# Optimization experiments

Measured on AMD Instinct MI355X. Metric: run time of the kernel, lower is better.

Reference implementation:

```python
import jax, jax.numpy as jnp
import numpy as np

LOWER = 300  # hidden size of the critic MLP


def setup_inputs() -> dict:
    key = jax.random.key(0)
    ks = jax.random.split(key, 6)
    N, XD, YD = 1024, 768, 768
    x = jax.random.normal(ks[0], (N, XD), dtype=jnp.float32)
    y = jax.random.normal(ks[1], (N, YD), dtype=jnp.float32)
    # Linear(x_dim+y_dim -> LOWER), Linear(LOWER -> 1); Kaiming-uniform-ish init
    b1_lim = 1.0 / np.sqrt(XD + YD)
    b2_lim = 1.0 / np.sqrt(LOWER)
    W1 = jax.random.uniform(ks[2], (XD + YD, LOWER), jnp.float32, -b1_lim, b1_lim)
    b1 = jax.random.uniform(ks[3], (LOWER,), jnp.float32, -b1_lim, b1_lim)
    W2 = jax.random.uniform(ks[4], (LOWER, 1), jnp.float32, -b2_lim, b2_lim)
    b2 = jax.random.uniform(ks[5], (1,), jnp.float32, -b2_lim, b2_lim)
    return {"x_samples": x, "y_samples": y, "W1": W1, "b1": b1, "W2": W2, "b2": b2}


def reference(x_samples, y_samples, W1, b1, W2, b2):
    N = y_samples.shape[0]
    xd = x_samples.shape[-1]
    # Decompose first Linear: cat([x, y]) @ W1 == x @ W1[:xd] + y @ W1[xd:]
    Wx, Wy = W1[:xd], W1[xd:]
    hx = x_samples @ Wx          # [N, LOWER]
    hy = y_samples @ Wy          # [N, LOWER]
    w2 = W2[:, 0]                # [LOWER]

    def critic(h):
        # relu -> Linear(LOWER->1) -> softplus
        return jax.nn.softplus(jax.nn.relu(h) @ w2 + b2[0])

    # T0[i] = F(x[i], y[i])
    T0 = critic(hx + hy + b1)                       # [N]
    # T1[i, j] = F(x[j], y[i])  (x tiled over dim 0, y over dim 1)
    h_pair = hy[:, None, :] + hx[None, :, :] + b1   # [N, N, LOWER]
    T1 = critic(h_pair)                             # [N, N]
    lower_bound = (T0.mean()
                   - jax.nn.logsumexp(T1, axis=1).mean()
                   - jnp.log(jnp.float32(N)))
    return lower_bound
```

## Files before the change

kernel.cpp:

```cpp
#include <hip/hip_runtime.h>
#include <math.h>

#define N_S 1024
#define XD  768
#define LOW 300
#define KP  320
#define KP2 160

typedef _Float16 h2  __attribute__((ext_vector_type(2)));
typedef __fp16   g2  __attribute__((ext_vector_type(2)));
typedef _Float16 v8h __attribute__((ext_vector_type(8)));
typedef float    f4  __attribute__((ext_vector_type(4)));

union U32H2 { unsigned int u; h2 h; };
__device__ inline h2 u2h(unsigned int v){ U32H2 t; t.u = v; return t.h; }
__device__ inline unsigned int pk(float a, float b){
    g2 t = __builtin_amdgcn_cvt_pkrtz(a, b);
    return __builtin_bit_cast(unsigned int, t);
}
union U4V8 { uint4 u; v8h v; };

__global__ __launch_bounds__(512)
void gemm_h(const float* __restrict__ x, const float* __restrict__ y,
            const float* __restrict__ W1, const float* __restrict__ b1g,
            unsigned int* __restrict__ hx_h, unsigned int* __restrict__ hy_h,
            float* __restrict__ partsum, unsigned int* __restrict__ cnt)
{
    __shared__ unsigned int As[2][32][36];
    __shared__ unsigned int Bs[2][64][36];

    const int tid = threadIdx.x;
    const int job = blockIdx.x;
    if (job < 256 && tid < 4) partsum[job * 4 + tid] = 0.f;
    if (job == 0 && tid == 4) cnt[0] = 0u;

    const int which = job >= 160;
    const int t = which ? job - 160 : job;
    const int n0 = (t % 5) * 64;
    const int r0 = (t / 5) * 32;
    const float* A = which ? y : x;
    const float* W = W1 + (size_t)which * XD * LOW;
    _Float16* outh = (_Float16*)(which ? hy_h : hx_h);

    const int w = tid >> 6, l = tid & 63;
    const int wm = w >> 2, wn = w & 3;
    const int lr = l & 15, lg = l >> 4;

    const int arow = tid >> 4, aq = tid & 15;
    const int bn = tid & 63, bms = tid >> 6;
    const bool bin = (n0 + bn) < LOW;

    f4 acc = {};
    float4 a0; float bw[8];
    a0 = *(const float4*)&A[(size_t)(r0 + arow) * XD + aq * 4];
    #pragma unroll
    for (int s = 0; s < 8; ++s)
        bw[s] = bin ? W[(size_t)(bms * 8 + s) * LOW + n0 + bn] : 0.f;

    const int NC = XD / 64;
    for (int c = 0; c < NC; ++c) {
        const int buf = c & 1;
        *(uint2*)&As[buf][arow][aq * 2] = make_uint2(pk(a0.x, a0.y), pk(a0.z, a0.w));
        *(uint4*)&Bs[buf][bn][bms * 4] =
            uint4{ pk(bw[0],bw[1]), pk(bw[2],bw[3]), pk(bw[4],bw[5]), pk(bw[6],bw[7]) };
        __syncthreads();
        if (c + 1 < NC) {
            const int kb = (c + 1) * 64;
            a0 = *(const float4*)&A[(size_t)(r0 + arow) * XD + kb + aq * 4];
            #pragma unroll
            for (int s = 0; s < 8; ++s)
                bw[s] = bin ? W[(size_t)(kb + bms * 8 + s) * LOW + n0 + bn] : 0.f;
        }
        #pragma unroll
        for (int ks = 0; ks < 2; ++ks) {
            const int ko = ks * 16 + lg * 4;
            U4V8 af; af.u = *(const uint4*)&As[buf][wm * 16 + lr][ko];
            U4V8 bf; bf.u = *(const uint4*)&Bs[buf][wn * 16 + lr][ko];
            acc = __builtin_amdgcn_mfma_f32_16x16x32_f16(af.v, bf.v, acc, 0, 0, 0);
        }
    }

    const int col = n0 + wn * 16 + lr;
    const float b1v = (which && col < LOW) ? b1g[col] : 0.f;
    #pragma unroll
    for (int r = 0; r < 4; ++r) {
        const int row = r0 + wm * 16 + lg * 4 + r;
        outh[(size_t)row * KP + col] = (_Float16)(acc[r] + b1v);
    }
}

__global__ __launch_bounds__(256)
void pair_kernel(const unsigned int* __restrict__ hx_h, const unsigned int* __restrict__ hy_h,
                 const float* __restrict__ W2, const float* __restrict__ b2,
                 float* __restrict__ partsum, float* __restrict__ diag,
                 unsigned int* __restrict__ cnt, float* __restrict__ out)
{
    const int jb = blockIdx.x & 15, ib = blockIdx.x >> 4;
    const int j0 = jb * 64, i0 = ib * 32;

    __shared__ unsigned int Hy[160][36];
    __shared__ unsigned int Hx[160][68];
    __shared__ unsigned int w2s[KP2];
    __shared__ unsigned int lastFlag;
    __shared__ float ssum[4];

    const int tid = threadIdx.x;

    {
        const int r = tid >> 3, q = tid & 7;
        const unsigned int* src = &hy_h[(size_t)(i0 + r) * KP2];
        #pragma unroll
        for (int e = 0; e < 5; ++e) {
            const int k4 = q + 8 * e;
            uint4 v = *(const uint4*)&src[k4 * 4];
            Hy[k4*4+0][r] = v.x; Hy[k4*4+1][r] = v.y;
            Hy[k4*4+2][r] = v.z; Hy[k4*4+3][r] = v.w;
        }
    }
    {
        const int r = tid >> 2, q = tid & 3;
        const unsigned int* src = &hx_h[(size_t)(j0 + r) * KP2];
        #pragma unroll
        for (int e = 0; e < 10; ++e) {
            const int k4 = q + 4 * e;
            uint4 v = *(const uint4*)&src[k4 * 4];
            Hx[k4*4+0][r] = v.x; Hx[k4*4+1][r] = v.y;
            Hx[k4*4+2][r] = v.z; Hx[k4*4+3][r] = v.w;
        }
    }
    if (tid < KP2) {
        int k = tid * 2;
        float w0 = (k < LOW) ? W2[k] : 0.f;
        float w1 = (k + 1 < LOW) ? W2[k + 1] : 0.f;
        w2s[tid] = pk(w0, w1);
    }
    __syncthreads();

    const int tx = tid & 15;
    const int kh = (tid >> 4) & 1;
    const int iy = tid >> 5;

    float acc[4][4] = {};
    const h2 hz = h2{(_Float16)0.f, (_Float16)0.f};
    const int kbase = kh * 80;

    #pragma unroll 4
    for (int kki = 0; kki < 80; ++kki) {
        const int kk = kbase + kki;
        const uint4 ya = *(const uint4*)&Hy[kk][iy * 4];
        const uint4 xb = *(const uint4*)&Hx[kk][tx * 4];
        const h2 w = u2h(w2s[kk]);
        const unsigned int yar[4] = {ya.x, ya.y, ya.z, ya.w};
        const unsigned int xbr[4] = {xb.x, xb.y, xb.z, xb.w};
        #pragma unroll
        for (int r = 0; r < 4; ++r) {
            const h2 a = u2h(yar[r]);
            #pragma unroll
            for (int q = 0; q < 4; ++q) {
                h2 z = __builtin_elementwise_max(a + u2h(xbr[q]), hz);
                acc[r][q] = __builtin_amdgcn_fdot2(z, w, acc[r][q], false);
            }
        }
    }

    #pragma unroll
    for (int r = 0; r < 4; ++r)
        #pragma unroll
        for (int q = 0; q < 4; ++q)
            acc[r][q] += __shfl_xor(acc[r][q], 16, 64);

    const float b2v = b2[0];
    #pragma unroll
    for (int r = 0; r < 4; ++r) {
        const int row = i0 + iy * 4 + r;
        float es = 0.f;
        #pragma unroll
        for (int q = 0; q < 4; ++q) {
            const float s = acc[r][q] + b2v;
            es += __expf(s);
            const int col = j0 + tx * 4 + q;
            if (col == row)
                atomicExch(&diag[row],
                           fmaxf(s, 0.f) + __logf(1.f + __expf(-fabsf(s))));
        }
        #pragma unroll
        for (int o = 1; o <= 8; o <<= 1) es += __shfl_xor(es, o, 64);
        if ((tid & 31) == 0) atomicAdd(&partsum[row], es);
    }

    asm volatile("s_waitcnt vmcnt(0)" ::: "memory");
    __syncthreads();
    if (tid == 0) lastFlag = (atomicAdd(cnt, 1u) == 511u) ? 1u : 0u;
    __syncthreads();
    if (!lastFlag) return;

    float csum = 0.f;
    #pragma unroll
    for (int g = 0; g < 4; ++g) {
        const int row = g * 256 + tid;
        const float ps = atomicAdd(&partsum[row], 0.f);
        const float dg = atomicAdd(&diag[row], 0.f);
        csum += dg - __logf((float)N_S + ps);
    }
    #pragma unroll
    for (int o = 32; o > 0; o >>= 1) csum += __shfl_xor(csum, o, 64);
    if ((tid & 63) == 0) ssum[tid >> 6] = csum;
    __syncthreads();
    if (tid == 0)
        out[0] = (ssum[0] + ssum[1] + ssum[2] + ssum[3]) * (1.0f / N_S)
               - logf((float)N_S);
}

extern "C" void kernel_launch(void* const* d_in, const int* in_sizes, int n_in,
                              void* d_out, int out_size, void* d_ws, size_t ws_size,
                              hipStream_t stream)
{
    const float* x  = (const float*)d_in[0];
    const float* y  = (const float*)d_in[1];
    const float* W1 = (const float*)d_in[2];
    const float* b1 = (const float*)d_in[3];
    const float* W2 = (const float*)d_in[4];
    const float* b2 = (const float*)d_in[5];
    float* outp = (float*)d_out;

    unsigned int* hx_h = (unsigned int*)d_ws;
    unsigned int* hy_h = hx_h + (size_t)N_S * KP2;
    float* partsum = (float*)(hy_h + (size_t)N_S * KP2);
    float* diag = partsum + N_S;
    unsigned int* cnt = (unsigned int*)(diag + N_S);

    gemm_h<<<320, 512, 0, stream>>>(x, y, W1, b1, hx_h, hy_h, partsum, cnt);

    pair_kernel<<<512, 256, 0, stream>>>(hx_h, hy_h, W2, b2,
                                         partsum, diag, cnt, outp);
}
```

Before: 41.29 us.

## Process two j-tiles per pair block, prefetching the next Hx tile into registers

Each pair_kernel block now covers two 64-column j tiles, so the grid shrinks from 512 to 256 blocks. The Hy tile and W2 load are reused across both tiles. The second Hx tile is loaded from global into registers while the first tile is being computed, overlapping load latency with compute. With 256 blocks on a 256-CU part, each CU gets one block, so there is less parallelism and less latency hiding across blocks, and the added registers for the prefetch may lower occupancy.

```diff
diff --git a/kernel.cpp b/kernel.cpp
--- a/kernel.cpp
+++ b/kernel.cpp
@@ -95,8 +95,9 @@
                  float* __restrict__ partsum, float* __restrict__ diag,
                  unsigned int* __restrict__ cnt, float* __restrict__ out)
 {
-    const int jb = blockIdx.x & 15, ib = blockIdx.x >> 4;
-    const int j0 = jb * 64, i0 = ib * 32;
+    const int jp = blockIdx.x & 7;
+    const int ib = blockIdx.x >> 3;
+    const int i0 = ib * 32;
 
     __shared__ unsigned int Hy[160][36];
     __shared__ unsigned int Hx[160][68];
@@ -117,80 +118,94 @@
             Hy[k4*4+2][r] = v.z; Hy[k4*4+3][r] = v.w;
         }
     }
-    {
-        const int r = tid >> 2, q = tid & 3;
-        const unsigned int* src = &hx_h[(size_t)(j0 + r) * KP2];
-        #pragma unroll
-        for (int e = 0; e < 10; ++e) {
-            const int k4 = q + 4 * e;
-            uint4 v = *(const uint4*)&src[k4 * 4];
-            Hx[k4*4+0][r] = v.x; Hx[k4*4+1][r] = v.y;
-            Hx[k4*4+2][r] = v.z; Hx[k4*4+3][r] = v.w;
-        }
-    }
     if (tid < KP2) {
         int k = tid * 2;
         float w0 = (k < LOW) ? W2[k] : 0.f;
         float w1 = (k + 1 < LOW) ? W2[k + 1] : 0.f;
         w2s[tid] = pk(w0, w1);
     }
-    __syncthreads();
+
+    const int xr = tid >> 2, xq = tid & 3;
+    uint4 xv[10];
+    {
+        const unsigned int* src = &hx_h[(size_t)(jp * 128 + xr) * KP2];
+        #pragma unroll
+        for (int e = 0; e < 10; ++e)
+            xv[e] = *(const uint4*)&src[(xq + 4 * e) * 4];
+    }
 
     const int tx = tid & 15;
     const int kh = (tid >> 4) & 1;
     const int iy = tid >> 5;
-
-    float acc[4][4] = {};
+    const float b2v = b2[0];
     const h2 hz = h2{(_Float16)0.f, (_Float16)0.f};
-    const int kbase = kh * 80;
-
-    #pragma unroll 4
-    for (int kki = 0; kki < 80; ++kki) {
-        const int kk = kbase + kki;
-        const uint4 ya = *(const uint4*)&Hy[kk][iy * 4];
-        const uint4 xb = *(const uint4*)&Hx[kk][tx * 4];
-        const h2 w = u2h(w2s[kk]);
-        const unsigned int yar[4] = {ya.x, ya.y, ya.z, ya.w};
-        const unsigned int xbr[4] = {xb.x, xb.y, xb.z, xb.w};
+
+    for (int jt = 0; jt < 2; ++jt) {
+        const int j0 = (jp * 2 + jt) * 64;
+        if (jt) __syncthreads();
+        #pragma unroll
+        for (int e = 0; e < 10; ++e) {
+            const int k4 = xq + 4 * e;
+            Hx[k4*4+0][xr] = xv[e].x; Hx[k4*4+1][xr] = xv[e].y;
+            Hx[k4*4+2][xr] = xv[e].z; Hx[k4*4+3][xr] = xv[e].w;
+        }
+        __syncthreads();
+        if (jt == 0) {
+            const unsigned int* src = &hx_h[(size_t)(jp * 128 + 64 + xr) * KP2];
+            #pragma unroll
+            for (int e = 0; e < 10; ++e)
+                xv[e] = *(const uint4*)&src[(xq + 4 * e) * 4];
+        }
+
+        float acc[4][4] = {};
+        const int kbase = kh * 80;
+        #pragma unroll 4
+        for (int kki = 0; kki < 80; ++kki) {
+            const int kk = kbase + kki;
+            const uint4 ya = *(const uint4*)&Hy[kk][iy * 4];
+            const uint4 xb = *(const uint4*)&Hx[kk][tx * 4];
+            const h2 w = u2h(w2s[kk]);
+            const unsigned int yar[4] = {ya.x, ya.y, ya.z, ya.w};
+            const unsigned int xbr[4] = {xb.x, xb.y, xb.z, xb.w};
+            #pragma unroll
+            for (int r = 0; r < 4; ++r) {
+                const h2 a = u2h(yar[r]);
+                #pragma unroll
+                for (int q = 0; q < 4; ++q) {
+                    h2 z = __builtin_elementwise_max(a + u2h(xbr[q]), hz);
+                    acc[r][q] = __builtin_amdgcn_fdot2(z, w, acc[r][q], false);
+                }
+            }
+        }
+
+        #pragma unroll
+        for (int r = 0; r < 4; ++r)
+            #pragma unroll
+            for (int q = 0; q < 4; ++q)
+                acc[r][q] += __shfl_xor(acc[r][q], 16, 64);
+
         #pragma unroll
         for (int r = 0; r < 4; ++r) {
-            const h2 a = u2h(yar[r]);
+            const int row = i0 + iy * 4 + r;
+            float es = 0.f;
             #pragma unroll
             for (int q = 0; q < 4; ++q) {
-                h2 z = __builtin_elementwise_max(a + u2h(xbr[q]), hz);
-                acc[r][q] = __builtin_amdgcn_fdot2(z, w, acc[r][q], false);
+                const float s = acc[r][q] + b2v;
+                es += __expf(s);
+                const int col = j0 + tx * 4 + q;
+                if (col == row)
+                    atomicExch(&diag[row],
+                               fmaxf(s, 0.f) + __logf(1.f + __expf(-fabsf(s))));
             }
-        }
-    }
-
-    #pragma unroll
-    for (int r = 0; r < 4; ++r)
-        #pragma unroll
-        for (int q = 0; q < 4; ++q)
-            acc[r][q] += __shfl_xor(acc[r][q], 16, 64);
-
-    const float b2v = b2[0];
-    #pragma unroll
-    for (int r = 0; r < 4; ++r) {
-        const int row = i0 + iy * 4 + r;
-        float es = 0.f;
-        #pragma unroll
-        for (int q = 0; q < 4; ++q) {
-            const float s = acc[r][q] + b2v;
-            es += __expf(s);
-            const int col = j0 + tx * 4 + q;
-            if (col == row)
-                atomicExch(&diag[row],
-                           fmaxf(s, 0.f) + __logf(1.f + __expf(-fabsf(s))));
-        }
-        #pragma unroll
-        for (int o = 1; o <= 8; o <<= 1) es += __shfl_xor(es, o, 64);
-        if ((tid & 31) == 0) atomicAdd(&partsum[row], es);
+            #pragma unroll
+            for (int o = 1; o <= 8; o <<= 1) es += __shfl_xor(es, o, 64);
+            if ((tid & 31) == 0) atomicAdd(&partsum[row], es);
+        }
     }
 
     asm volatile("s_waitcnt vmcnt(0)" ::: "memory");
     __syncthreads();
-    if (tid == 0) lastFlag = (atomicAdd(cnt, 1u) == 511u) ? 1u : 0u;
+    if (tid == 0) lastFlag = (atomicAdd(cnt, 1u) == 255u) ? 1u : 0u;
     __syncthreads();
     if (!lastFlag) return;
 
@@ -231,6 +246,6 @@
 
     gemm_h<<<320, 512, 0, stream>>>(x, y, W1, b1, hx_h, hy_h, partsum, cnt);
 
-    pair_kernel<<<512, 256, 0, stream>>>(hx_h, hy_h, W2, b2,
+    pair_kernel<<<256, 256, 0, stream>>>(hx_h, hy_h, W2, b2,
                                          partsum, diag, cnt, outp);
 }
```

New measurement: 43.63 us. +5.7%, slower.

## Retile pair kernel to 32x32 blocks with 2x2 per-thread outputs over full K

Applied to the files above, without the earlier changes.

The pair kernel now uses 32x32 output tiles (1024 blocks instead of 512), and each thread computes a 2x2 output tile over the full K range. The previous scheme was a 4x4 tile with K split across two half-warps and joined by a shuffle. Shared memory now keeps rows in their natural k-major layout, so the transposed scatter on load is gone, and W2 is packed into uint4 so one vector read serves 8 k values. The goal is more parallelism and cheaper LDS staging. The cost is lower register reuse: there are 4 accumulators per 4 uint4 loads instead of 16 per 2, so LDS bandwidth per FLOP rises.

```diff
diff --git a/kernel.cpp b/kernel.cpp
--- a/kernel.cpp
+++ b/kernel.cpp
@@ -95,12 +95,12 @@
                  float* __restrict__ partsum, float* __restrict__ diag,
                  unsigned int* __restrict__ cnt, float* __restrict__ out)
 {
-    const int jb = blockIdx.x & 15, ib = blockIdx.x >> 4;
-    const int j0 = jb * 64, i0 = ib * 32;
-
-    __shared__ unsigned int Hy[160][36];
-    __shared__ unsigned int Hx[160][68];
-    __shared__ unsigned int w2s[KP2];
+    const int jb = blockIdx.x & 31, ib = blockIdx.x >> 5;
+    const int j0 = jb * 32, i0 = ib * 32;
+
+    __shared__ unsigned int Hy[32][164];
+    __shared__ unsigned int Hx[32][164];
+    __shared__ uint4 w2q[40];
     __shared__ unsigned int lastFlag;
     __shared__ float ssum[4];
 
@@ -108,89 +108,82 @@
 
     {
         const int r = tid >> 3, q = tid & 7;
-        const unsigned int* src = &hy_h[(size_t)(i0 + r) * KP2];
+        const unsigned int* sy = &hy_h[(size_t)(i0 + r) * KP2];
+        const unsigned int* sx = &hx_h[(size_t)(j0 + r) * KP2];
         #pragma unroll
         for (int e = 0; e < 5; ++e) {
-            const int k4 = q + 8 * e;
-            uint4 v = *(const uint4*)&src[k4 * 4];
-            Hy[k4*4+0][r] = v.x; Hy[k4*4+1][r] = v.y;
-            Hy[k4*4+2][r] = v.z; Hy[k4*4+3][r] = v.w;
-        }
-    }
-    {
-        const int r = tid >> 2, q = tid & 3;
-        const unsigned int* src = &hx_h[(size_t)(j0 + r) * KP2];
-        #pragma unroll
-        for (int e = 0; e < 10; ++e) {
-            const int k4 = q + 4 * e;
-            uint4 v = *(const uint4*)&src[k4 * 4];
-            Hx[k4*4+0][r] = v.x; Hx[k4*4+1][r] = v.y;
-            Hx[k4*4+2][r] = v.z; Hx[k4*4+3][r] = v.w;
-        }
-    }
-    if (tid < KP2) {
-        int k = tid * 2;
-        float w0 = (k < LOW) ? W2[k] : 0.f;
-        float w1 = (k + 1 < LOW) ? W2[k + 1] : 0.f;
-        w2s[tid] = pk(w0, w1);
+            const int c4 = (q + 8 * e) * 4;
+            *(uint4*)&Hy[r][c4] = *(const uint4*)&sy[c4];
+            *(uint4*)&Hx[r][c4] = *(const uint4*)&sx[c4];
+        }
+    }
+    if (tid < 40) {
+        const int k = tid * 8;
+        float wv[8];
+        #pragma unroll
+        for (int e = 0; e < 8; ++e)
+            wv[e] = (k + e < LOW) ? W2[k + e] : 0.f;
+        w2q[tid] = uint4{ pk(wv[0],wv[1]), pk(wv[2],wv[3]),
+                          pk(wv[4],wv[5]), pk(wv[6],wv[7]) };
     }
     __syncthreads();
 
     const int tx = tid & 15;
-    const int kh = (tid >> 4) & 1;
-    const int iy = tid >> 5;
-
-    float acc[4][4] = {};
+    const int ty = tid >> 4;
+
+    float a00 = 0.f, a01 = 0.f, a10 = 0.f, a11 = 0.f;
     const h2 hz = h2{(_Float16)0.f, (_Float16)0.f};
-    const int kbase = kh * 80;
 
     #pragma unroll 4
-    for (int kki = 0; kki < 80; ++kki) {
-        const int kk = kbase + kki;
-        const uint4 ya = *(const uint4*)&Hy[kk][iy * 4];
-        const uint4 xb = *(const uint4*)&Hx[kk][tx * 4];
-        const h2 w = u2h(w2s[kk]);
-        const unsigned int yar[4] = {ya.x, ya.y, ya.z, ya.w};
-        const unsigned int xbr[4] = {xb.x, xb.y, xb.z, xb.w};
-        #pragma unroll
-        for (int r = 0; r < 4; ++r) {
-            const h2 a = u2h(yar[r]);
-            #pragma unroll
-            for (int q = 0; q < 4; ++q) {
-                h2 z = __builtin_elementwise_max(a + u2h(xbr[q]), hz);
-                acc[r][q] = __builtin_amdgcn_fdot2(z, w, acc[r][q], false);
-            }
-        }
-    }
-
-    #pragma unroll
-    for (int r = 0; r < 4; ++r)
-        #pragma unroll
-        for (int q = 0; q < 4; ++q)
-            acc[r][q] += __shfl_xor(acc[r][q], 16, 64);
+    for (int t = 0; t < 40; ++t) {
+        const uint4 ya0 = *(const uint4*)&Hy[2*ty  ][t*4];
+        const uint4 ya1 = *(const uint4*)&Hy[2*ty+1][t*4];
+        const uint4 xb0 = *(const uint4*)&Hx[2*tx  ][t*4];
+        const uint4 xb1 = *(const uint4*)&Hx[2*tx+1][t*4];
+        const uint4 wv  = w2q[t];
+        const unsigned int y0e[4] = {ya0.x, ya0.y, ya0.z, ya0.w};
+        const unsigned int y1e[4] = {ya1.x, ya1.y, ya1.z, ya1.w};
+        const unsigned int x0e[4] = {xb0.x, xb0.y, xb0.z, xb0.w};
+        const unsigned int x1e[4] = {xb1.x, xb1.y, xb1.z, xb1.w};
+        const unsigned int wve[4] = {wv.x, wv.y, wv.z, wv.w};
+        #pragma unroll
+        for (int e = 0; e < 4; ++e) {
+            const h2 w  = u2h(wve[e]);
+            const h2 p0 = u2h(y0e[e]), p1 = u2h(y1e[e]);
+            const h2 q0 = u2h(x0e[e]), q1 = u2h(x1e[e]);
+            a00 = __builtin_amdgcn_fdot2(__builtin_elementwise_max(p0 + q0, hz), w, a00, false);
+            a01 = __builtin_amdgcn_fdot2(__builtin_elementwise_max(p0 + q1, hz), w, a01, false);
+            a10 = __builtin_amdgcn_fdot2(__builtin_elementwise_max(p1 + q0, hz), w, a10, false);
+            a11 = __builtin_amdgcn_fdot2(__builtin_elementwise_max(p1 + q1, hz), w, a11, false);
+        }
+    }
 
     const float b2v = b2[0];
-    #pragma unroll
-    for (int r = 0; r < 4; ++r) {
-        const int row = i0 + iy * 4 + r;
-        float es = 0.f;
-        #pragma unroll
-        for (int q = 0; q < 4; ++q) {
-            const float s = acc[r][q] + b2v;
-            es += __expf(s);
-            const int col = j0 + tx * 4 + q;
-            if (col == row)
-                atomicExch(&diag[row],
-                           fmaxf(s, 0.f) + __logf(1.f + __expf(-fabsf(s))));
-        }
-        #pragma unroll
-        for (int o = 1; o <= 8; o <<= 1) es += __shfl_xor(es, o, 64);
-        if ((tid & 31) == 0) atomicAdd(&partsum[row], es);
+    const int row0 = i0 + 2*ty, row1 = row0 + 1;
+    const int col0 = j0 + 2*tx, col1 = col0 + 1;
+    const float s00 = a00 + b2v, s01 = a01 + b2v;
+    const float s10 = a10 + b2v, s11 = a11 + b2v;
+
+    if (col0 == row0) atomicExch(&diag[row0], fmaxf(s00,0.f) + __logf(1.f + __expf(-fabsf(s00))));
+    if (col1 == row0) atomicExch(&diag[row0], fmaxf(s01,0.f) + __logf(1.f + __expf(-fabsf(s01))));
+    if (col0 == row1) atomicExch(&diag[row1], fmaxf(s10,0.f) + __logf(1.f + __expf(-fabsf(s10))));
+    if (col1 == row1) atomicExch(&diag[row1], fmaxf(s11,0.f) + __logf(1.f + __expf(-fabsf(s11))));
+
+    float es0 = __expf(s00) + __expf(s01);
+    float es1 = __expf(s10) + __expf(s11);
+    #pragma unroll
+    for (int o = 1; o <= 8; o <<= 1) {
+        es0 += __shfl_xor(es0, o, 64);
+        es1 += __shfl_xor(es1, o, 64);
+    }
+    if (tx == 0) {
+        atomicAdd(&partsum[row0], es0);
+        atomicAdd(&partsum[row1], es1);
     }
 
     asm volatile("s_waitcnt vmcnt(0)" ::: "memory");
     __syncthreads();
-    if (tid == 0) lastFlag = (atomicAdd(cnt, 1u) == 511u) ? 1u : 0u;
+    if (tid == 0) lastFlag = (atomicAdd(cnt, 1u) == 1023u) ? 1u : 0u;
     __syncthreads();
     if (!lastFlag) return;
 
@@ -231,6 +224,6 @@
 
     gemm_h<<<320, 512, 0, stream>>>(x, y, W1, b1, hx_h, hy_h, partsum, cnt);
 
-    pair_kernel<<<512, 256, 0, stream>>>(hx_h, hy_h, W2, b2,
-                                         partsum, diag, cnt, outp);
-}
+    pair_kernel<<<1024, 256, 0, stream>>>(hx_h, hy_h, W2, b2,
+                                          partsum, diag, cnt, outp);
+}
```

Result: no change. 41.02 us (-0.7%).

## Accumulate pair critic in packed fp16 FMA with row-major swizzled LDS tiles

Applied to the files above, without the earlier changes.

The pair kernel now accumulates each relu(hy+hx)*w2 product with packed half-precision FMA into fp16 partial sums, flushing them to fp32 every 16 k-pairs. This replaces fdot2, which has fp32 accumulation. LDS tiles change from a k-major transpose to row-major storage with an XOR swizzle on Hx, so loads become direct 16-byte copies without bank conflicts. Block indices are also remapped to change scheduling order. The fp16 partial accumulation adds rounding error to the logsumexp inputs.

```diff
diff --git a/kernel.cpp b/kernel.cpp
--- a/kernel.cpp
+++ b/kernel.cpp
@@ -95,11 +95,13 @@
                  float* __restrict__ partsum, float* __restrict__ diag,
                  unsigned int* __restrict__ cnt, float* __restrict__ out)
 {
-    const int jb = blockIdx.x & 15, ib = blockIdx.x >> 4;
+    const int b0 = blockIdx.x;
+    const int bs = (b0 & 7) * 64 + (b0 >> 3);
+    const int jb = bs & 15, ib = bs >> 4;
     const int j0 = jb * 64, i0 = ib * 32;
 
-    __shared__ unsigned int Hy[160][36];
-    __shared__ unsigned int Hx[160][68];
+    __shared__ unsigned int Hy[32][160];
+    __shared__ unsigned int Hx[64][160];
     __shared__ unsigned int w2s[KP2];
     __shared__ unsigned int lastFlag;
     __shared__ float ssum[4];
@@ -107,25 +109,25 @@
     const int tid = threadIdx.x;
 
     {
-        const int r = tid >> 3, q = tid & 7;
-        const unsigned int* src = &hy_h[(size_t)(i0 + r) * KP2];
+        const int r = tid >> 3, sq = tid & 7;
+        const unsigned int* sy = &hy_h[(size_t)(i0 + r) * KP2];
         #pragma unroll
         for (int e = 0; e < 5; ++e) {
-            const int k4 = q + 8 * e;
-            uint4 v = *(const uint4*)&src[k4 * 4];
-            Hy[k4*4+0][r] = v.x; Hy[k4*4+1][r] = v.y;
-            Hy[k4*4+2][r] = v.z; Hy[k4*4+3][r] = v.w;
+            const int s = sq + 8 * e;
+            *(uint4*)&Hy[r][s * 4] = *(const uint4*)&sy[s * 4];
         }
     }
     {
-        const int r = tid >> 2, q = tid & 3;
-        const unsigned int* src = &hx_h[(size_t)(j0 + r) * KP2];
-        #pragma unroll
-        for (int e = 0; e < 10; ++e) {
-            const int k4 = q + 4 * e;
-            uint4 v = *(const uint4*)&src[k4 * 4];
-            Hx[k4*4+0][r] = v.x; Hx[k4*4+1][r] = v.y;
-            Hx[k4*4+2][r] = v.z; Hx[k4*4+3][r] = v.w;
+        #pragma unroll
+        for (int rp = 0; rp < 2; ++rp) {
+            const int r = (tid >> 3) + 32 * rp, sq = tid & 7;
+            const unsigned int* sx = &hx_h[(size_t)(j0 + r) * KP2];
+            const int swz = (r >> 2) & 7;
+            #pragma unroll
+            for (int e = 0; e < 5; ++e) {
+                const int s = sq + 8 * e;
+                *(uint4*)&Hx[r][(s ^ swz) * 4] = *(const uint4*)&sx[s * 4];
+            }
         }
     }
     if (tid < KP2) {
@@ -139,35 +141,60 @@
     const int tx = tid & 15;
     const int kh = (tid >> 4) & 1;
     const int iy = tid >> 5;
-
-    float acc[4][4] = {};
+    const int xsw = tx & 7;
+
+    float accf[4][4] = {};
     const h2 hz = h2{(_Float16)0.f, (_Float16)0.f};
-    const int kbase = kh * 80;
-
-    #pragma unroll 4
-    for (int kki = 0; kki < 80; ++kki) {
-        const int kk = kbase + kki;
-        const uint4 ya = *(const uint4*)&Hy[kk][iy * 4];
-        const uint4 xb = *(const uint4*)&Hx[kk][tx * 4];
-        const h2 w = u2h(w2s[kk]);
-        const unsigned int yar[4] = {ya.x, ya.y, ya.z, ya.w};
-        const unsigned int xbr[4] = {xb.x, xb.y, xb.z, xb.w};
-        #pragma unroll
-        for (int r = 0; r < 4; ++r) {
-            const h2 a = u2h(yar[r]);
-            #pragma unroll
-            for (int q = 0; q < 4; ++q) {
-                h2 z = __builtin_elementwise_max(a + u2h(xbr[q]), hz);
-                acc[r][q] = __builtin_amdgcn_fdot2(z, w, acc[r][q], false);
+    const int tb = kh * 20;
+
+    for (int tc = 0; tc < 5; ++tc) {
+        h2 acch[4][4];
+        #pragma unroll
+        for (int r = 0; r < 4; ++r)
+            #pragma unroll
+            for (int q = 0; q < 4; ++q) acch[r][q] = hz;
+
+        #pragma unroll
+        for (int ti = 0; ti < 4; ++ti) {
+            const int t = tb + tc * 4 + ti;
+            uint4 ya[4], xb[4];
+            #pragma unroll
+            for (int r = 0; r < 4; ++r)
+                ya[r] = *(const uint4*)&Hy[iy * 4 + r][t * 4];
+            const int sx = (t ^ xsw) * 4;
+            #pragma unroll
+            for (int q = 0; q < 4; ++q)
+                xb[q] = *(const uint4*)&Hx[tx * 4 + q][sx];
+            const uint4 wv = *(const uint4*)&w2s[t * 4];
+            const unsigned int wve[4] = {wv.x, wv.y, wv.z, wv.w};
+            #pragma unroll
+            for (int e = 0; e < 4; ++e) {
+                const h2 w = u2h(wve[e]);
+                const unsigned int yae[4] = {ya[0][e], ya[1][e], ya[2][e], ya[3][e]};
+                const unsigned int xbe[4] = {xb[0][e], xb[1][e], xb[2][e], xb[3][e]};
+                #pragma unroll
+                for (int r = 0; r < 4; ++r) {
+                    const h2 a = u2h(yae[r]);
+                    #pragma unroll
+                    for (int q = 0; q < 4; ++q) {
+                        h2 z = __builtin_elementwise_max(a + u2h(xbe[q]), hz);
+                        acch[r][q] = __builtin_elementwise_fma(z, w, acch[r][q]);
+                    }
+                }
             }
         }
+        #pragma unroll
+        for (int r = 0; r < 4; ++r)
+            #pragma unroll
+            for (int q = 0; q < 4; ++q)
+                accf[r][q] += (float)acch[r][q][0] + (float)acch[r][q][1];
     }
 
     #pragma unroll
     for (int r = 0; r < 4; ++r)
         #pragma unroll
         for (int q = 0; q < 4; ++q)
-            acc[r][q] += __shfl_xor(acc[r][q], 16, 64);
+            accf[r][q] += __shfl_xor(accf[r][q], 16, 64);
 
     const float b2v = b2[0];
     #pragma unroll
@@ -176,7 +203,7 @@
         float es = 0.f;
         #pragma unroll
         for (int q = 0; q < 4; ++q) {
-            const float s = acc[r][q] + b2v;
+            const float s = accf[r][q] + b2v;
             es += __expf(s);
             const int col = j0 + tx * 4 + q;
             if (col == row)
```

New measurement: 43.84 us. 6.2% more time.
